# Kernel tuning notes

Measured on AMD Instinct MI355X. Metric: run time of the kernel, lower is better.

Reference implementation:

```python
import jax, jax.numpy as jnp
import numpy as np
import math

D_MODEL, H, D_FF = 1024, 16, 4096
B, S = 4, 2048
EPS = 1e-6

def layer_norm(x, alpha, beta):
    # Faithful to torch: x.std uses Bessel correction (ddof=1), eps added to std.
    mean = jnp.mean(x, axis=-1, keepdims=True)
    std = jnp.std(x, axis=-1, keepdims=True, ddof=1)
    return alpha * (x - mean) / (std + EPS) + beta

def setup_inputs() -> dict:
    key = jax.random.key(0)
    ks = jax.random.split(key, 8)
    sc = 0.02
    return {
        "x": jax.random.normal(ks[0], (B, S, D_MODEL), jnp.float32),
        "mask": jnp.ones((B, 1, 1, S), jnp.int32),
        "wq": jax.random.normal(ks[1], (D_MODEL, D_MODEL), jnp.float32) * sc,
        "wk": jax.random.normal(ks[2], (D_MODEL, D_MODEL), jnp.float32) * sc,
        "wv": jax.random.normal(ks[3], (D_MODEL, D_MODEL), jnp.float32) * sc,
        "wo": jax.random.normal(ks[4], (D_MODEL, D_MODEL), jnp.float32) * sc,
        "w1": jax.random.normal(ks[5], (D_MODEL, D_FF), jnp.float32) * sc,
        "b1": jnp.zeros((D_FF,), jnp.float32),
        "w2": jax.random.normal(ks[6], (D_FF, D_MODEL), jnp.float32) * sc,
        "b2": jnp.zeros((D_MODEL,), jnp.float32),
        "ln1_a": jnp.ones((D_MODEL,), jnp.float32),
        "ln1_b": jnp.zeros((D_MODEL,), jnp.float32),
        "ln2_a": jnp.ones((D_MODEL,), jnp.float32),
        "ln2_b": jnp.zeros((D_MODEL,), jnp.float32),
    }

def mha(xn, mask, wq, wk, wv, wo):
    b, s, d = xn.shape
    d_k = d // H
    q = (xn @ wq).reshape(b, s, H, d_k).transpose(0, 2, 1, 3)  # [B,H,S,dk]
    k = (xn @ wk).reshape(b, s, H, d_k).transpose(0, 2, 1, 3)
    v = (xn @ wv).reshape(b, s, H, d_k).transpose(0, 2, 1, 3)
    scores = jnp.einsum('bhqd,bhkd->bhqk', q, k) / math.sqrt(d_k)
    scores = jnp.where(mask == 0, -1e9, scores)
    attn = jax.nn.softmax(scores, axis=-1)
    out = jnp.einsum('bhqk,bhkd->bhqd', attn, v)
    out = out.transpose(0, 2, 1, 3).reshape(b, s, d)
    return out @ wo

def reference(x, mask, wq, wk, wv, wo, w1, b1, w2, b2, ln1_a, ln1_b, ln2_a, ln2_b):
    # Pre-LN residual 1: self-attention (dropout=0 / eval mode -> identity)
    xn = layer_norm(x, ln1_a, ln1_b)
    x = x + mha(xn, mask, wq, wk, wv, wo)
    # Pre-LN residual 2: FFN
    xn = layer_norm(x, ln2_a, ln2_b)
    ff = jax.nn.relu(xn @ w1 + b1) @ w2 + b2
    return x + ff
```

## Files before the change

### kernel.cpp

```cpp
#include <hip/hip_runtime.h>
#include <hip/hip_bf16.h>

typedef __bf16 bf16x8 __attribute__((ext_vector_type(8)));
typedef __bf16 bf16x4 __attribute__((ext_vector_type(4)));
typedef float  f32x4  __attribute__((ext_vector_type(4)));

#define MFMA(a, b, c) __builtin_amdgcn_mfma_f32_16x16x32_bf16((a), (b), (c), 0, 0, 0)

__device__ inline unsigned int pkbf(float a, float b) {
    __bf16 x = (__bf16)a, y = (__bf16)b;
    return (unsigned int)*(unsigned short*)&x |
           ((unsigned int)*(unsigned short*)&y << 16);
}

__global__ __launch_bounds__(256) void transpose_cvt(
    const float* __restrict__ src, __bf16* __restrict__ dst, int Kd, int Nd)
{
    __shared__ float tile[32][33];
    const int k0 = blockIdx.y * 32, n0 = blockIdx.x * 32;
    const int t = threadIdx.x;
    const int r = t >> 5, c = t & 31;
#pragma unroll
    for (int i = 0; i < 4; ++i)
        tile[r + i * 8][c] = src[(long)(k0 + r + i * 8) * Nd + n0 + c];
    __syncthreads();
#pragma unroll
    for (int i = 0; i < 4; ++i)
        dst[(long)(n0 + r + i * 8) * Kd + k0 + c] = (__bf16)tile[c][r + i * 8];
}

__global__ __launch_bounds__(256) void transpose_v(
    const __bf16* __restrict__ V, __bf16* __restrict__ Vt)
{
    __shared__ __bf16 tile[32][33];
    const int bh = blockIdx.z;
    const int s0 = blockIdx.x * 32, d0 = blockIdx.y * 32;
    const int t = threadIdx.x, r = t >> 5, c = t & 31;
    const __bf16* Vp = V + (long)bh * 2048 * 64;
    __bf16* Tp = Vt + (long)bh * 64 * 2048;
#pragma unroll
    for (int i = 0; i < 4; ++i)
        tile[r + i * 8][c] = Vp[(long)(s0 + r + i * 8) * 64 + d0 + c];
    __syncthreads();
#pragma unroll
    for (int i = 0; i < 4; ++i)
        Tp[(long)(d0 + r + i * 8) * 2048 + s0 + c] = tile[c][r + i * 8];
}

__global__ __launch_bounds__(256) void ln_kernel(
    const float* __restrict__ in, const float* __restrict__ ga,
    const float* __restrict__ gb, __bf16* __restrict__ out)
{
    const int row = blockIdx.x;
    const int t = threadIdx.x;
    const float4 xv = *(const float4*)(in + (long)row * 1024 + t * 4);
    float s  = xv.x + xv.y + xv.z + xv.w;
    float sq = xv.x * xv.x + xv.y * xv.y + xv.z * xv.z + xv.w * xv.w;
#pragma unroll
    for (int off = 32; off; off >>= 1) {
        s  += __shfl_xor(s, off);
        sq += __shfl_xor(sq, off);
    }
    __shared__ float red[8];
    const int w = t >> 6;
    if ((t & 63) == 0) { red[w * 2] = s; red[w * 2 + 1] = sq; }
    __syncthreads();
    s  = red[0] + red[2] + red[4] + red[6];
    sq = red[1] + red[3] + red[5] + red[7];
    const float mean = s * (1.0f / 1024.0f);
    const float var  = fmaxf((sq - s * mean) * (1.0f / 1023.0f), 0.0f);
    const float dinv = 1.0f / (sqrtf(var) + 1e-6f);
    const float4 av = *(const float4*)(ga + t * 4);
    const float4 bv = *(const float4*)(gb + t * 4);
    bf16x4 o;
    o[0] = (__bf16)((xv.x - mean) * dinv * av.x + bv.x);
    o[1] = (__bf16)((xv.y - mean) * dinv * av.y + bv.y);
    o[2] = (__bf16)((xv.z - mean) * dinv * av.z + bv.z);
    o[3] = (__bf16)((xv.w - mean) * dinv * av.w + bv.w);
    *(bf16x4*)(out + (long)row * 1024 + t * 4) = o;
}

template <int MODE>
__global__ __launch_bounds__(256) void gemm_bt(
    const __bf16* __restrict__ A, const __bf16* __restrict__ Bt,
    int M, int N, int K,
    const float* __restrict__ bias, const float* resid,
    float* outf, __bf16* __restrict__ outb,
    __bf16* __restrict__ qb, __bf16* __restrict__ kb, __bf16* __restrict__ vb)
{
    __shared__ __align__(16) __bf16 Alds[2][128 * 32];
    __shared__ __align__(16) __bf16 Blds[2][128 * 32];

    const int t = threadIdx.x;
    const int lane = t & 63, w = t >> 6;
    const int wr = w >> 1, wc = w & 1;
    const int g = lane >> 4, l15 = lane & 15;

    const int nwg = gridDim.x * gridDim.y;
    const int hwid = blockIdx.y * gridDim.x + blockIdx.x;
    const int wid = (hwid & 7) * (nwg >> 3) + (hwid >> 3);
    const int bm = (wid / gridDim.x) * 128;
    const int bn = (wid % gridDim.x) * 128;

    const int cr = t >> 2;
    const int cc = (t & 3) * 8;
    const __bf16* Ag  = A  + (long)(bm + cr) * K + cc;
    const __bf16* Ag2 = Ag + (long)64 * K;
    const __bf16* Bg  = Bt + (long)(bn + cr) * K + cc;
    const __bf16* Bg2 = Bg + (long)64 * K;
    const int wof = cr * 32 + cc;

    f32x4 acc[4][4] = {};
    const int nk = K / 32;

    bf16x8 ra0 = *(const bf16x8*)(Ag);
    bf16x8 ra1 = *(const bf16x8*)(Ag2);
    bf16x8 rb0 = *(const bf16x8*)(Bg);
    bf16x8 rb1 = *(const bf16x8*)(Bg2);
    *(bf16x8*)(&Alds[0][wof])           = ra0;
    *(bf16x8*)(&Alds[0][wof + 64 * 32]) = ra1;
    *(bf16x8*)(&Blds[0][wof])           = rb0;
    *(bf16x8*)(&Blds[0][wof + 64 * 32]) = rb1;
    ra0 = *(const bf16x8*)(Ag  + 32);
    ra1 = *(const bf16x8*)(Ag2 + 32);
    rb0 = *(const bf16x8*)(Bg  + 32);
    rb1 = *(const bf16x8*)(Bg2 + 32);
    __syncthreads();

    for (int kt = 0; kt < nk; ++kt) {
        const int cur = kt & 1;
        if (kt + 1 < nk) {
            *(bf16x8*)(&Alds[cur ^ 1][wof])           = ra0;
            *(bf16x8*)(&Alds[cur ^ 1][wof + 64 * 32]) = ra1;
            *(bf16x8*)(&Blds[cur ^ 1][wof])           = rb0;
            *(bf16x8*)(&Blds[cur ^ 1][wof + 64 * 32]) = rb1;
            if (kt + 2 < nk) {
                const long ko = (long)(kt + 2) * 32;
                ra0 = *(const bf16x8*)(Ag  + ko);
                ra1 = *(const bf16x8*)(Ag2 + ko);
                rb0 = *(const bf16x8*)(Bg  + ko);
                rb1 = *(const bf16x8*)(Bg2 + ko);
            }
        }
        const __bf16* Ab = &Alds[cur][0];
        const __bf16* Bb = &Blds[cur][0];
        bf16x8 af[4], bfr[4];
#pragma unroll
        for (int mi = 0; mi < 4; ++mi)
            af[mi] = *(const bf16x8*)(Ab + (wr * 64 + mi * 16 + l15) * 32 + g * 8);
#pragma unroll
        for (int ni = 0; ni < 4; ++ni)
            bfr[ni] = *(const bf16x8*)(Bb + (wc * 64 + ni * 16 + l15) * 32 + g * 8);
#pragma unroll
        for (int mi = 0; mi < 4; ++mi)
#pragma unroll
            for (int ni = 0; ni < 4; ++ni)
                acc[mi][ni] = MFMA(af[mi], bfr[ni], acc[mi][ni]);
        __syncthreads();
    }

#pragma unroll
    for (int mi = 0; mi < 4; ++mi) {
#pragma unroll
        for (int ni = 0; ni < 4; ++ni) {
#pragma unroll
            for (int r = 0; r < 4; ++r) {
                const int gr = bm + wr * 64 + mi * 16 + g * 4 + r;
                const int gc = bn + wc * 64 + ni * 16 + l15;
                const float vacc = acc[mi][ni][r];
                if constexpr (MODE == 0) {
                    const int bufi = gc >> 10;
                    const int hd = gc & 1023;
                    const int h = hd >> 6, d = hd & 63;
                    const int b = gr >> 11, sx = gr & 2047;
                    __bf16* dst = (bufi == 0) ? qb : ((bufi == 1) ? kb : vb);
                    dst[((long)((b * 16 + h) * 2048 + sx)) * 64 + d] = (__bf16)vacc;
                } else if constexpr (MODE == 1) {
                    const long idx = (long)gr * N + gc;
                    outf[idx] = vacc + resid[idx];
                } else if constexpr (MODE == 2) {
                    const float y = fmaxf(vacc + bias[gc], 0.0f);
                    outb[(long)gr * N + gc] = (__bf16)y;
                } else {
                    const long idx = (long)gr * N + gc;
                    outf[idx] = vacc + bias[gc] + resid[idx];
                }
            }
        }
    }
}

__global__ __launch_bounds__(256, 2) void attn_kernel(
    const __bf16* __restrict__ Q, const __bf16* __restrict__ Kk,
    const __bf16* __restrict__ Vt, const int* __restrict__ mask,
    __bf16* __restrict__ O)
{
    __shared__ __align__(16) char Klds[8192];
    __shared__ __align__(16) char Vlds[8192];
    __shared__ int mlds[64];
    __shared__ int tflag[32];

    const int t = threadIdx.x;
    const int lane = t & 63, w = t >> 6;
    const int g = lane >> 4, l15 = lane & 15;
    const int bh = blockIdx.x >> 4;
    const int qt = blockIdx.x & 15;
    const int b = bh >> 4, h = bh & 15;
    const int q0 = qt * 128 + w * 32;

    const __bf16* Qp = Q  + (long)bh * 2048 * 64;
    const __bf16* Kp = Kk + (long)bh * 2048 * 64;
    const __bf16* Vp = Vt + (long)bh * 64 * 2048;
    const int* mp = mask + b * 2048;

    {
        const int4* mi4 = (const int4*)(mp + t * 8);
        const int4 ma = mi4[0], mb = mi4[1];
        const int ok = (ma.x && ma.y && ma.z && ma.w &&
                        mb.x && mb.y && mb.z && mb.w) ? 1 : 0;
        const unsigned long long bal = __ballot(ok);
        if ((lane & 7) == 0)
            tflag[t >> 3] = (((bal >> lane) & 0xFFull) == 0xFFull) ? 1 : 0;
    }

    bf16x8 qreg[2][2];
#pragma unroll
    for (int qf = 0; qf < 2; ++qf)
#pragma unroll
        for (int kh = 0; kh < 2; ++kh)
            qreg[qf][kh] = *(const bf16x8*)(Qp + (long)(q0 + qf * 16 + l15) * 64 + kh * 32 + g * 8);

    bf16x8 vone;
#pragma unroll
    for (int j = 0; j < 8; ++j) vone[j] = (__bf16)1.0f;

    const float Csc = 0.18033688011112042f;
    float m2_run[2] = {-1e30f, -1e30f};
    f32x4 la[2] = {};
    f32x4 ot[2][4] = {};

    const int sr0 = t >> 3;
    const int sce = (t & 7) * 8;
    const int swz0 = sr0 * 128 + (((t & 7) * 16) ^ ((sr0 & 7) << 4));
    const int swz1 = swz0 + 32 * 128;

    bf16x8 kr0 = *(const bf16x8*)(Kp + (long)sr0 * 64 + sce);
    bf16x8 kr1 = *(const bf16x8*)(Kp + (long)(sr0 + 32) * 64 + sce);
    bf16x8 vr0 = *(const bf16x8*)(Vp + (long)sr0 * 2048 + sce);
    bf16x8 vr1 = *(const bf16x8*)(Vp + (long)(sr0 + 32) * 2048 + sce);
    int mr = (t < 64) ? mp[t] : 0;

    for (int kc = 0; kc < 32; ++kc) {
        __syncthreads();
        *(bf16x8*)(Klds + swz0) = kr0;
        *(bf16x8*)(Klds + swz1) = kr1;
        *(bf16x8*)(Vlds + swz0) = vr0;
        *(bf16x8*)(Vlds + swz1) = vr1;
        if (t < 64) mlds[t] = mr;
        __syncthreads();
        if (kc < 31) {
            const int kv0 = (kc + 1) * 64;
            kr0 = *(const bf16x8*)(Kp + (long)(kv0 + sr0) * 64 + sce);
            kr1 = *(const bf16x8*)(Kp + (long)(kv0 + sr0 + 32) * 64 + sce);
            vr0 = *(const bf16x8*)(Vp + (long)sr0 * 2048 + kv0 + sce);
            vr1 = *(const bf16x8*)(Vp + (long)(sr0 + 32) * 2048 + kv0 + sce);
            if (t < 64) mr = mp[kv0 + t];
        }
        const bool fullv = (tflag[kc] != 0);

        bf16x8 kf[4][2];
#pragma unroll
        for (int f = 0; f < 4; ++f)
#pragma unroll
            for (int dh = 0; dh < 2; ++dh)
                kf[f][dh] = *(const bf16x8*)(Klds + (f * 16 + l15) * 128 +
                                             ((dh * 64 + g * 16) ^ ((l15 & 7) << 4)));
        f32x4 sf[2][4] = {};
        __builtin_amdgcn_s_setprio(1);
#pragma unroll
        for (int qf = 0; qf < 2; ++qf)
#pragma unroll
            for (int f = 0; f < 4; ++f) {
                sf[qf][f] = MFMA(kf[f][0], qreg[qf][0], sf[qf][f]);
                sf[qf][f] = MFMA(kf[f][1], qreg[qf][1], sf[qf][f]);
            }
        __builtin_amdgcn_s_setprio(0);

        bf16x8 av[4][2];
#pragma unroll
        for (int df = 0; df < 4; ++df) {
            const int row = (df * 16 + l15) * 128;
            const int sx = (l15 & 7) << 4;
#pragma unroll
            for (int hh = 0; hh < 2; ++hh) {
                const bf16x4 lo = *(const bf16x4*)(Vlds + row + ((hh * 64 + g * 8) ^ sx));
                const bf16x4 hi = *(const bf16x4*)(Vlds + row + ((hh * 64 + 32 + g * 8) ^ sx));
                bf16x8 a;
                a[0] = lo[0]; a[1] = lo[1]; a[2] = lo[2]; a[3] = lo[3];
                a[4] = hi[0]; a[5] = hi[1]; a[6] = hi[2]; a[7] = hi[3];
                av[df][hh] = a;
            }
        }

#pragma unroll
        for (int qf = 0; qf < 2; ++qf) {
            float s[16];
            if (fullv) {
#pragma unroll
                for (int i = 0; i < 16; ++i) s[i] = sf[qf][i >> 2][i & 3];
            } else {
                int mvv[16];
#pragma unroll
                for (int f = 0; f < 4; ++f) {
                    const int4 mq = *(const int4*)&mlds[f * 16 + g * 4];
                    mvv[f * 4 + 0] = mq.x; mvv[f * 4 + 1] = mq.y;
                    mvv[f * 4 + 2] = mq.z; mvv[f * 4 + 3] = mq.w;
                }
#pragma unroll
                for (int i = 0; i < 16; ++i)
                    s[i] = (mvv[i] == 0) ? -1e9f : sf[qf][i >> 2][i & 3];
            }
            float m01 = fmaxf(s[0], s[1]),   m23 = fmaxf(s[2], s[3]);
            float m45 = fmaxf(s[4], s[5]),   m67 = fmaxf(s[6], s[7]);
            float m89 = fmaxf(s[8], s[9]),   mab = fmaxf(s[10], s[11]);
            float mcd = fmaxf(s[12], s[13]), mef = fmaxf(s[14], s[15]);
            float mx = fmaxf(fmaxf(fmaxf(m01, m23), fmaxf(m45, m67)),
                             fmaxf(fmaxf(m89, mab), fmaxf(mcd, mef)));
            mx = fmaxf(mx, __shfl_xor(mx, 16));
            mx = fmaxf(mx, __shfl_xor(mx, 32));
            const float m2 = mx * Csc;
            if (!__all(m2 - m2_run[qf] <= 8.0f)) {
                const float m2n = fmaxf(m2_run[qf], m2);
                const float alpha = __builtin_amdgcn_exp2f(m2_run[qf] - m2n);
#pragma unroll
                for (int r = 0; r < 4; ++r) la[qf][r] *= alpha;
#pragma unroll
                for (int df = 0; df < 4; ++df)
#pragma unroll
                    for (int r = 0; r < 4; ++r) ot[qf][df][r] *= alpha;
                m2_run[qf] = m2n;
            }
            const float nm2 = -m2_run[qf];
            float p[16];
#pragma unroll
            for (int i = 0; i < 16; ++i)
                p[i] = __builtin_amdgcn_exp2f(__builtin_fmaf(s[i], Csc, nm2));

#pragma unroll
            for (int hh = 0; hh < 2; ++hh) {
                unsigned int pu[4] = {pkbf(p[hh * 8 + 0], p[hh * 8 + 1]),
                                      pkbf(p[hh * 8 + 2], p[hh * 8 + 3]),
                                      pkbf(p[hh * 8 + 4], p[hh * 8 + 5]),
                                      pkbf(p[hh * 8 + 6], p[hh * 8 + 7])};
                bf16x8 pf = *(bf16x8*)pu;
                __builtin_amdgcn_s_setprio(1);
#pragma unroll
                for (int df = 0; df < 4; ++df)
                    ot[qf][df] = MFMA(av[df][hh], pf, ot[qf][df]);
                la[qf] = MFMA(vone, pf, la[qf]);
                __builtin_amdgcn_s_setprio(0);
            }
        }
    }

#pragma unroll
    for (int qf = 0; qf < 2; ++qf) {
        const float inv = 1.0f / la[qf][0];
        const int q = q0 + qf * 16 + l15;
        __bf16* orow = O + (long)(b * 2048 + q) * 1024 + h * 64;
#pragma unroll
        for (int df = 0; df < 4; ++df)
#pragma unroll
            for (int rp = 0; rp < 2; ++rp) {
                const int d = df * 16 + g * 4 + rp * 2;
                *(unsigned int*)(orow + d) =
                    pkbf(ot[qf][df][rp * 2] * inv, ot[qf][df][rp * 2 + 1] * inv);
            }
    }
}

extern "C" void kernel_launch(void* const* d_in, const int* in_sizes, int n_in,
                              void* d_out, int out_size, void* d_ws, size_t ws_size,
                              hipStream_t stream)
{
    const float* x    = (const float*)d_in[0];
    const int*   mask = (const int*)  d_in[1];
    const float* wq   = (const float*)d_in[2];
    const float* wk   = (const float*)d_in[3];
    const float* wv   = (const float*)d_in[4];
    const float* wo   = (const float*)d_in[5];
    const float* w1   = (const float*)d_in[6];
    const float* b1   = (const float*)d_in[7];
    const float* w2   = (const float*)d_in[8];
    const float* b2   = (const float*)d_in[9];
    const float* l1a  = (const float*)d_in[10];
    const float* l1b  = (const float*)d_in[11];
    const float* l2a  = (const float*)d_in[12];
    const float* l2b  = (const float*)d_in[13];
    float* out = (float*)d_out;

    char* ws = (char*)d_ws;
    __bf16* wqkvT = (__bf16*)(ws);
    __bf16* woT   = (__bf16*)(ws + 6291456);
    __bf16* w1T   = (__bf16*)(ws + 8388608);
    __bf16* w2T   = (__bf16*)(ws + 16777216);
    __bf16* xn    = (__bf16*)(ws + 25165824);
    __bf16* Vtb   = (__bf16*)(ws + 25165824);
    __bf16* Qb    = (__bf16*)(ws + 41943040);
    __bf16* Kb    = (__bf16*)(ws + 58720256);
    __bf16* Vb    = (__bf16*)(ws + 75497472);
    __bf16* attO  = (__bf16*)(ws + 92274688);
    __bf16* ffh   = (__bf16*)(ws + 41943040);

    transpose_cvt<<<dim3(32, 32),  256, 0, stream>>>(wq, wqkvT,               1024, 1024);
    transpose_cvt<<<dim3(32, 32),  256, 0, stream>>>(wk, wqkvT + 1024 * 1024, 1024, 1024);
    transpose_cvt<<<dim3(32, 32),  256, 0, stream>>>(wv, wqkvT + 2048 * 1024, 1024, 1024);
    transpose_cvt<<<dim3(32, 32),  256, 0, stream>>>(wo, woT,                 1024, 1024);
    transpose_cvt<<<dim3(128, 32), 256, 0, stream>>>(w1, w1T,                 1024, 4096);
    transpose_cvt<<<dim3(32, 128), 256, 0, stream>>>(w2, w2T,                 4096, 1024);

    ln_kernel<<<8192, 256, 0, stream>>>(x, l1a, l1b, xn);
    gemm_bt<0><<<dim3(24, 64), 256, 0, stream>>>(xn, wqkvT, 8192, 3072, 1024,
                                                 nullptr, nullptr, nullptr, nullptr, Qb, Kb, Vb);
    transpose_v<<<dim3(64, 2, 64), 256, 0, stream>>>(Vb, Vtb);
    attn_kernel<<<1024, 256, 0, stream>>>(Qb, Kb, Vtb, mask, attO);
    gemm_bt<1><<<dim3(8, 64), 256, 0, stream>>>(attO, woT, 8192, 1024, 1024,
                                                nullptr, x, out, nullptr, nullptr, nullptr, nullptr);
    ln_kernel<<<8192, 256, 0, stream>>>(out, l2a, l2b, xn);
    gemm_bt<2><<<dim3(32, 64), 256, 0, stream>>>(xn, w1T, 8192, 4096, 1024,
                                                 b1, nullptr, nullptr, ffh, nullptr, nullptr, nullptr);
    gemm_bt<3><<<dim3(8, 64), 256, 0, stream>>>(ffh, w2T, 8192, 1024, 4096,
                                                b2, out, out, nullptr, nullptr, nullptr, nullptr);
    (void)in_sizes; (void)n_in; (void)out_size; (void)ws_size;
}
```

Measured before the change: 456.4 us.

## Add 256x256 tile GEMM with direct global-to-LDS loads for QKV and FFN1

Adds a new 512-thread GEMM kernel with 256x256 output tiles, a 64-wide K step, XOR-swizzled LDS layout filled by global_load_lds (bypassing registers), double buffering, and MFMA priority raising. It replaces the 128x128 kernel for the QKV projection and the first FFN matmul, aiming to raise arithmetic intensity and cut global/LDS traffic. It uses 128KB of LDS per block, which limits occupancy and leaves fewer blocks than CUs for the QKV grid (384 blocks), so tail effects may appear.

```diff
diff --git a/kernel.cpp b/kernel.cpp
--- a/kernel.cpp
+++ b/kernel.cpp
@@ -6,6 +6,10 @@
 typedef float  f32x4  __attribute__((ext_vector_type(4)));
 
 #define MFMA(a, b, c) __builtin_amdgcn_mfma_f32_16x16x32_bf16((a), (b), (c), 0, 0, 0)
+
+#define GLOAD16(gp, lp) __builtin_amdgcn_global_load_lds(                      \
+    (const __attribute__((address_space(1))) void*)(gp),                       \
+    (__attribute__((address_space(3))) void*)(lp), 16, 0, 0)
 
 __device__ inline unsigned int pkbf(float a, float b) {
     __bf16 x = (__bf16)a, y = (__bf16)b;
@@ -81,12 +85,114 @@
 }
 
 template <int MODE>
+__global__ __launch_bounds__(512, 2) void gemm256(
+    const __bf16* __restrict__ A, const __bf16* __restrict__ Bt,
+    int M, int N, int K,
+    const float* __restrict__ bias, __bf16* __restrict__ outb,
+    __bf16* __restrict__ qb, __bf16* __restrict__ kb2, __bf16* __restrict__ vb)
+{
+    __shared__ __align__(16) char LDS[131072];
+
+    const int t = threadIdx.x;
+    const int lane = t & 63;
+    const int g = lane >> 4, l15 = lane & 15;
+    const int wid = t >> 6;
+    const int wm = wid >> 2, wn = wid & 3;
+
+    const int nwg = gridDim.x * gridDim.y;
+    const int hwid = blockIdx.y * gridDim.x + blockIdx.x;
+    const int swid = (hwid & 7) * (nwg >> 3) + (hwid >> 3);
+    const int bm = (swid / gridDim.x) * 256;
+    const int bn = (swid % gridDim.x) * 256;
+
+    int r1, kb1, r2, kbb2;
+    { const int p = t >> 3, sv = (t & 7) ^ (p & 7);
+      r1 = 2 * p + ((sv >> 2) & 1); kb1 = (sv & 3) * 16; }
+    { const int c = t + 512, p = c >> 3, sv = (c & 7) ^ (p & 7);
+      r2 = 2 * p + ((sv >> 2) & 1); kbb2 = (sv & 3) * 16; }
+    const char* a1 = (const char*)A  + ((long)(bm + r1) * K) * 2 + kb1;
+    const char* a2 = (const char*)A  + ((long)(bm + r2) * K) * 2 + kbb2;
+    const char* b1 = (const char*)Bt + ((long)(bn + r1) * K) * 2 + kb1;
+    const char* b2 = (const char*)Bt + ((long)(bn + r2) * K) * 2 + kbb2;
+    char* const dA1 = LDS + t * 16;
+    char* const dA2 = LDS + 8192 + t * 16;
+    char* const dB1 = LDS + 65536 + t * 16;
+    char* const dB2 = LDS + 65536 + 8192 + t * 16;
+
+#define STG(kt, kh, buf) do {                                                  \
+        const long go_ = (long)(kt) * 128 + (kh) * 64;                         \
+        const int lo_ = (buf) * 32768 + (kh) * 16384;                          \
+        GLOAD16(a1 + go_, dA1 + lo_); GLOAD16(a2 + go_, dA2 + lo_);            \
+        GLOAD16(b1 + go_, dB1 + lo_); GLOAD16(b2 + go_, dB2 + lo_); } while (0)
+
+    const int ph = l15 >> 1;
+    const int slot = ((((l15 & 1) << 2) | g) ^ ph) << 4;
+    const int aoff = wm * 8192 + ph * 128 + slot;
+    const int boff = 65536 + wn * 4096 + ph * 128 + slot;
+
+    f32x4 acc[8][4] = {};
+    const int nt = K / 64;
+
+    STG(0, 0, 0);
+    STG(0, 1, 0);
+
+    for (int kt = 0; kt < nt; ++kt) {
+        const int cur = kt & 1;
+#pragma unroll
+        for (int kh = 0; kh < 2; ++kh) {
+            asm volatile("s_waitcnt vmcnt(4)" ::: "memory");
+            asm volatile("s_barrier" ::: "memory");
+            if (kt + 1 < nt) STG(kt + 1, kh, cur ^ 1);
+            const char* pl = LDS + cur * 32768 + kh * 16384;
+            bf16x8 af[8], bfr[4];
+#pragma unroll
+            for (int ni = 0; ni < 4; ++ni)
+                bfr[ni] = *(const bf16x8*)(pl + boff + ni * 1024);
+#pragma unroll
+            for (int mi = 0; mi < 8; ++mi)
+                af[mi] = *(const bf16x8*)(pl + aoff + mi * 1024);
+            __builtin_amdgcn_s_setprio(1);
+#pragma unroll
+            for (int mi = 0; mi < 8; ++mi)
+#pragma unroll
+                for (int ni = 0; ni < 4; ++ni)
+                    acc[mi][ni] = MFMA(af[mi], bfr[ni], acc[mi][ni]);
+            __builtin_amdgcn_s_setprio(0);
+        }
+    }
+#undef STG
+
+#pragma unroll
+    for (int mi = 0; mi < 8; ++mi) {
+#pragma unroll
+        for (int ni = 0; ni < 4; ++ni) {
+#pragma unroll
+            for (int r = 0; r < 4; ++r) {
+                const int gr = bm + wm * 128 + mi * 16 + g * 4 + r;
+                const int gc = bn + wn * 64 + ni * 16 + l15;
+                const float v = acc[mi][ni][r];
+                if constexpr (MODE == 0) {
+                    const int bufi = gc >> 10;
+                    const int hd = gc & 1023;
+                    const int h = hd >> 6, d = hd & 63;
+                    const int b = gr >> 11, sx = gr & 2047;
+                    __bf16* dst = (bufi == 0) ? qb : ((bufi == 1) ? kb2 : vb);
+                    dst[((long)((b * 16 + h) * 2048 + sx)) * 64 + d] = (__bf16)v;
+                } else {
+                    const float y = fmaxf(v + bias[gc], 0.0f);
+                    outb[(long)gr * N + gc] = (__bf16)y;
+                }
+            }
+        }
+    }
+}
+
+template <int MODE>
 __global__ __launch_bounds__(256) void gemm_bt(
     const __bf16* __restrict__ A, const __bf16* __restrict__ Bt,
     int M, int N, int K,
     const float* __restrict__ bias, const float* resid,
-    float* outf, __bf16* __restrict__ outb,
-    __bf16* __restrict__ qb, __bf16* __restrict__ kb, __bf16* __restrict__ vb)
+    float* outf, __bf16* __restrict__ outb)
 {
     __shared__ __align__(16) __bf16 Alds[2][128 * 32];
     __shared__ __align__(16) __bf16 Blds[2][128 * 32];
@@ -168,19 +274,9 @@
                 const int gr = bm + wr * 64 + mi * 16 + g * 4 + r;
                 const int gc = bn + wc * 64 + ni * 16 + l15;
                 const float vacc = acc[mi][ni][r];
-                if constexpr (MODE == 0) {
-                    const int bufi = gc >> 10;
-                    const int hd = gc & 1023;
-                    const int h = hd >> 6, d = hd & 63;
-                    const int b = gr >> 11, sx = gr & 2047;
-                    __bf16* dst = (bufi == 0) ? qb : ((bufi == 1) ? kb : vb);
-                    dst[((long)((b * 16 + h) * 2048 + sx)) * 64 + d] = (__bf16)vacc;
-                } else if constexpr (MODE == 1) {
+                if constexpr (MODE == 1) {
                     const long idx = (long)gr * N + gc;
                     outf[idx] = vacc + resid[idx];
-                } else if constexpr (MODE == 2) {
-                    const float y = fmaxf(vacc + bias[gc], 0.0f);
-                    outb[(long)gr * N + gc] = (__bf16)y;
                 } else {
                     const long idx = (long)gr * N + gc;
                     outf[idx] = vacc + bias[gc] + resid[idx];
@@ -420,16 +516,16 @@
     transpose_cvt<<<dim3(32, 128), 256, 0, stream>>>(w2, w2T,                 4096, 1024);
 
     ln_kernel<<<8192, 256, 0, stream>>>(x, l1a, l1b, xn);
-    gemm_bt<0><<<dim3(24, 64), 256, 0, stream>>>(xn, wqkvT, 8192, 3072, 1024,
-                                                 nullptr, nullptr, nullptr, nullptr, Qb, Kb, Vb);
+    gemm256<0><<<dim3(12, 32), 512, 0, stream>>>(xn, wqkvT, 8192, 3072, 1024,
+                                                 nullptr, nullptr, Qb, Kb, Vb);
     transpose_v<<<dim3(64, 2, 64), 256, 0, stream>>>(Vb, Vtb);
     attn_kernel<<<1024, 256, 0, stream>>>(Qb, Kb, Vtb, mask, attO);
     gemm_bt<1><<<dim3(8, 64), 256, 0, stream>>>(attO, woT, 8192, 1024, 1024,
-                                                nullptr, x, out, nullptr, nullptr, nullptr, nullptr);
+                                                nullptr, x, out, nullptr);
     ln_kernel<<<8192, 256, 0, stream>>>(out, l2a, l2b, xn);
-    gemm_bt<2><<<dim3(32, 64), 256, 0, stream>>>(xn, w1T, 8192, 4096, 1024,
-                                                 b1, nullptr, nullptr, ffh, nullptr, nullptr, nullptr);
+    gemm256<2><<<dim3(16, 32), 512, 0, stream>>>(xn, w1T, 8192, 4096, 1024,
+                                                 b1, ffh, nullptr, nullptr, nullptr);
     gemm_bt<3><<<dim3(8, 64), 256, 0, stream>>>(ffh, w2T, 8192, 1024, 4096,
-                                                b2, out, out, nullptr, nullptr, nullptr, nullptr);
+                                                b2, out, out, nullptr);
     (void)in_sizes; (void)n_in; (void)out_size; (void)ws_size;
 }
```

After: 462.0 us. About the same (+1.2%).

## Double-buffer attention K/V tiles and software-pipeline QK^T; merge square weight transposes

Applied to the files above, without the earlier changes.

The attention kernel now keeps two LDS buffers for K, V and the mask. It computes the QK^T scores for the next tile before running softmax and PV on the current one, so MFMA work on the next tile can overlap the exp and softmax work on the current tile. The cost is twice the LDS footprint and a second set of score registers, which may reduce occupancy at two blocks per CU. Separately, the four 1024x1024 weight transpose-convert launches are merged into one launch using a z grid dimension, cutting launch overhead.

```diff
diff --git a/kernel.cpp b/kernel.cpp
--- a/kernel.cpp
+++ b/kernel.cpp
@@ -11,6 +11,28 @@
     __bf16 x = (__bf16)a, y = (__bf16)b;
     return (unsigned int)*(unsigned short*)&x |
            ((unsigned int)*(unsigned short*)&y << 16);
+}
+
+__global__ __launch_bounds__(256) void transpose_cvt4(
+    const float* __restrict__ s0, const float* __restrict__ s1,
+    const float* __restrict__ s2, const float* __restrict__ s3,
+    __bf16* __restrict__ d0, __bf16* __restrict__ d1,
+    __bf16* __restrict__ d2, __bf16* __restrict__ d3)
+{
+    __shared__ float tile[32][33];
+    const int z = blockIdx.z;
+    const float* src = (z == 0) ? s0 : (z == 1) ? s1 : (z == 2) ? s2 : s3;
+    __bf16* dst = (z == 0) ? d0 : (z == 1) ? d1 : (z == 2) ? d2 : d3;
+    const int k0 = blockIdx.y * 32, n0 = blockIdx.x * 32;
+    const int t = threadIdx.x;
+    const int r = t >> 5, c = t & 31;
+#pragma unroll
+    for (int i = 0; i < 4; ++i)
+        tile[r + i * 8][c] = src[(long)(k0 + r + i * 8) * 1024 + n0 + c];
+    __syncthreads();
+#pragma unroll
+    for (int i = 0; i < 4; ++i)
+        dst[(long)(n0 + r + i * 8) * 1024 + k0 + c] = (__bf16)tile[c][r + i * 8];
 }
 
 __global__ __launch_bounds__(256) void transpose_cvt(
@@ -195,9 +217,9 @@
     const __bf16* __restrict__ Vt, const int* __restrict__ mask,
     __bf16* __restrict__ O)
 {
-    __shared__ __align__(16) char Klds[8192];
-    __shared__ __align__(16) char Vlds[8192];
-    __shared__ int mlds[64];
+    __shared__ __align__(16) char Klds[2][8192];
+    __shared__ __align__(16) char Vlds[2][8192];
+    __shared__ int mlds[2][64];
     __shared__ int tflag[32];
 
     const int t = threadIdx.x;
@@ -249,43 +271,86 @@
     bf16x8 vr0 = *(const bf16x8*)(Vp + (long)sr0 * 2048 + sce);
     bf16x8 vr1 = *(const bf16x8*)(Vp + (long)(sr0 + 32) * 2048 + sce);
     int mr = (t < 64) ? mp[t] : 0;
-
-    for (int kc = 0; kc < 32; ++kc) {
-        __syncthreads();
-        *(bf16x8*)(Klds + swz0) = kr0;
-        *(bf16x8*)(Klds + swz1) = kr1;
-        *(bf16x8*)(Vlds + swz0) = vr0;
-        *(bf16x8*)(Vlds + swz1) = vr1;
-        if (t < 64) mlds[t] = mr;
-        __syncthreads();
-        if (kc < 31) {
-            const int kv0 = (kc + 1) * 64;
-            kr0 = *(const bf16x8*)(Kp + (long)(kv0 + sr0) * 64 + sce);
-            kr1 = *(const bf16x8*)(Kp + (long)(kv0 + sr0 + 32) * 64 + sce);
-            vr0 = *(const bf16x8*)(Vp + (long)sr0 * 2048 + kv0 + sce);
-            vr1 = *(const bf16x8*)(Vp + (long)(sr0 + 32) * 2048 + kv0 + sce);
-            if (t < 64) mr = mp[kv0 + t];
+    *(bf16x8*)(Klds[0] + swz0) = kr0;
+    *(bf16x8*)(Klds[0] + swz1) = kr1;
+    *(bf16x8*)(Vlds[0] + swz0) = vr0;
+    *(bf16x8*)(Vlds[0] + swz1) = vr1;
+    if (t < 64) mlds[0][t] = mr;
+    kr0 = *(const bf16x8*)(Kp + (long)(64 + sr0) * 64 + sce);
+    kr1 = *(const bf16x8*)(Kp + (long)(64 + sr0 + 32) * 64 + sce);
+    vr0 = *(const bf16x8*)(Vp + (long)sr0 * 2048 + 64 + sce);
+    vr1 = *(const bf16x8*)(Vp + (long)(sr0 + 32) * 2048 + 64 + sce);
+    mr = (t < 64) ? mp[64 + t] : 0;
+    __syncthreads();
+
+    f32x4 sfA[2][4], sfB[2][4];
+    {
+#pragma unroll
+        for (int qf = 0; qf < 2; ++qf)
+#pragma unroll
+            for (int f = 0; f < 4; ++f) sfA[qf][f] = (f32x4){};
+        bf16x8 kf[4][2];
+#pragma unroll
+        for (int f = 0; f < 4; ++f)
+#pragma unroll
+            for (int dh = 0; dh < 2; ++dh)
+                kf[f][dh] = *(const bf16x8*)(Klds[0] + (f * 16 + l15) * 128 +
+                                             ((dh * 64 + g * 16) ^ ((l15 & 7) << 4)));
+        __builtin_amdgcn_s_setprio(1);
+#pragma unroll
+        for (int qf = 0; qf < 2; ++qf)
+#pragma unroll
+            for (int f = 0; f < 4; ++f) {
+                sfA[qf][f] = MFMA(kf[f][0], qreg[qf][0], sfA[qf][f]);
+                sfA[qf][f] = MFMA(kf[f][1], qreg[qf][1], sfA[qf][f]);
+            }
+        __builtin_amdgcn_s_setprio(0);
+    }
+
+    auto process = [&](int KC, f32x4 (&SFU)[2][4], f32x4 (&SFN)[2][4]) {
+        const int cur = KC & 1;
+        if (KC < 31) {
+            __syncthreads();
+            char* Kn = Klds[cur ^ 1];
+            char* Vn = Vlds[cur ^ 1];
+            *(bf16x8*)(Kn + swz0) = kr0;
+            *(bf16x8*)(Kn + swz1) = kr1;
+            *(bf16x8*)(Vn + swz0) = vr0;
+            *(bf16x8*)(Vn + swz1) = vr1;
+            if (t < 64) mlds[cur ^ 1][t] = mr;
+            __syncthreads();
+            if (KC < 30) {
+                const int kv0 = (KC + 2) * 64;
+                kr0 = *(const bf16x8*)(Kp + (long)(kv0 + sr0) * 64 + sce);
+                kr1 = *(const bf16x8*)(Kp + (long)(kv0 + sr0 + 32) * 64 + sce);
+                vr0 = *(const bf16x8*)(Vp + (long)sr0 * 2048 + kv0 + sce);
+                vr1 = *(const bf16x8*)(Vp + (long)(sr0 + 32) * 2048 + kv0 + sce);
+                if (t < 64) mr = mp[kv0 + t];
+            }
+#pragma unroll
+            for (int qf = 0; qf < 2; ++qf)
+#pragma unroll
+                for (int f = 0; f < 4; ++f) SFN[qf][f] = (f32x4){};
+            bf16x8 kf[4][2];
+#pragma unroll
+            for (int f = 0; f < 4; ++f)
+#pragma unroll
+                for (int dh = 0; dh < 2; ++dh)
+                    kf[f][dh] = *(const bf16x8*)(Kn + (f * 16 + l15) * 128 +
+                                                 ((dh * 64 + g * 16) ^ ((l15 & 7) << 4)));
+            __builtin_amdgcn_s_setprio(1);
+#pragma unroll
+            for (int qf = 0; qf < 2; ++qf)
+#pragma unroll
+                for (int f = 0; f < 4; ++f) {
+                    SFN[qf][f] = MFMA(kf[f][0], qreg[qf][0], SFN[qf][f]);
+                    SFN[qf][f] = MFMA(kf[f][1], qreg[qf][1], SFN[qf][f]);
+                }
+            __builtin_amdgcn_s_setprio(0);
         }
-        const bool fullv = (tflag[kc] != 0);
-
-        bf16x8 kf[4][2];
-#pragma unroll
-        for (int f = 0; f < 4; ++f)
-#pragma unroll
-            for (int dh = 0; dh < 2; ++dh)
-                kf[f][dh] = *(const bf16x8*)(Klds + (f * 16 + l15) * 128 +
-                                             ((dh * 64 + g * 16) ^ ((l15 & 7) << 4)));
-        f32x4 sf[2][4] = {};
-        __builtin_amdgcn_s_setprio(1);
-#pragma unroll
-        for (int qf = 0; qf < 2; ++qf)
-#pragma unroll
-            for (int f = 0; f < 4; ++f) {
-                sf[qf][f] = MFMA(kf[f][0], qreg[qf][0], sf[qf][f]);
-                sf[qf][f] = MFMA(kf[f][1], qreg[qf][1], sf[qf][f]);
-            }
-        __builtin_amdgcn_s_setprio(0);
-
+
+        const bool fullv = (tflag[KC] != 0);
+        const char* Vc = Vlds[cur];
         bf16x8 av[4][2];
 #pragma unroll
         for (int df = 0; df < 4; ++df) {
@@ -293,8 +358,8 @@
             const int sx = (l15 & 7) << 4;
 #pragma unroll
             for (int hh = 0; hh < 2; ++hh) {
-                const bf16x4 lo = *(const bf16x4*)(Vlds + row + ((hh * 64 + g * 8) ^ sx));
-                const bf16x4 hi = *(const bf16x4*)(Vlds + row + ((hh * 64 + 32 + g * 8) ^ sx));
+                const bf16x4 lo = *(const bf16x4*)(Vc + row + ((hh * 64 + g * 8) ^ sx));
+                const bf16x4 hi = *(const bf16x4*)(Vc + row + ((hh * 64 + 32 + g * 8) ^ sx));
                 bf16x8 a;
                 a[0] = lo[0]; a[1] = lo[1]; a[2] = lo[2]; a[3] = lo[3];
                 a[4] = hi[0]; a[5] = hi[1]; a[6] = hi[2]; a[7] = hi[3];
@@ -307,18 +372,18 @@
             float s[16];
             if (fullv) {
 #pragma unroll
-                for (int i = 0; i < 16; ++i) s[i] = sf[qf][i >> 2][i & 3];
+                for (int i = 0; i < 16; ++i) s[i] = SFU[qf][i >> 2][i & 3];
             } else {
                 int mvv[16];
 #pragma unroll
                 for (int f = 0; f < 4; ++f) {
-                    const int4 mq = *(const int4*)&mlds[f * 16 + g * 4];
+                    const int4 mq = *(const int4*)&mlds[cur][f * 16 + g * 4];
                     mvv[f * 4 + 0] = mq.x; mvv[f * 4 + 1] = mq.y;
                     mvv[f * 4 + 2] = mq.z; mvv[f * 4 + 3] = mq.w;
                 }
 #pragma unroll
                 for (int i = 0; i < 16; ++i)
-                    s[i] = (mvv[i] == 0) ? -1e9f : sf[qf][i >> 2][i & 3];
+                    s[i] = (mvv[i] == 0) ? -1e9f : SFU[qf][i >> 2][i & 3];
             }
             float m01 = fmaxf(s[0], s[1]),   m23 = fmaxf(s[2], s[3]);
             float m45 = fmaxf(s[4], s[5]),   m67 = fmaxf(s[6], s[7]);
@@ -361,6 +426,11 @@
                 __builtin_amdgcn_s_setprio(0);
             }
         }
+    };
+
+    for (int kc = 0; kc < 32; kc += 2) {
+        process(kc,     sfA, sfB);
+        process(kc + 1, sfB, sfA);
     }
 
 #pragma unroll
@@ -412,12 +482,10 @@
     __bf16* attO  = (__bf16*)(ws + 92274688);
     __bf16* ffh   = (__bf16*)(ws + 41943040);
 
-    transpose_cvt<<<dim3(32, 32),  256, 0, stream>>>(wq, wqkvT,               1024, 1024);
-    transpose_cvt<<<dim3(32, 32),  256, 0, stream>>>(wk, wqkvT + 1024 * 1024, 1024, 1024);
-    transpose_cvt<<<dim3(32, 32),  256, 0, stream>>>(wv, wqkvT + 2048 * 1024, 1024, 1024);
-    transpose_cvt<<<dim3(32, 32),  256, 0, stream>>>(wo, woT,                 1024, 1024);
-    transpose_cvt<<<dim3(128, 32), 256, 0, stream>>>(w1, w1T,                 1024, 4096);
-    transpose_cvt<<<dim3(32, 128), 256, 0, stream>>>(w2, w2T,                 4096, 1024);
+    transpose_cvt4<<<dim3(32, 32, 4), 256, 0, stream>>>(
+        wq, wk, wv, wo, wqkvT, wqkvT + 1024 * 1024, wqkvT + 2048 * 1024, woT);
+    transpose_cvt<<<dim3(128, 32), 256, 0, stream>>>(w1, w1T, 1024, 4096);
+    transpose_cvt<<<dim3(32, 128), 256, 0, stream>>>(w2, w2T, 4096, 1024);
 
     ln_kernel<<<8192, 256, 0, stream>>>(x, l1a, l1b, xn);
     gemm_bt<0><<<dim3(24, 64), 256, 0, stream>>>(xn, wqkvT, 8192, 3072, 1024,
```

Result: no change. 452.8 us (-0.8%).
